# Kernel tuning notes

Measured on AMD Instinct MI355X. Metric: run time of the kernel, lower is better.

Reference implementation:

```python
import jax, jax.numpy as jnp
import numpy as np

K = 3  # spatial window (window_size = [1,3,3,1])


def _extract_patches(x, k):
    """TF-style extract_patches, VALID padding, stride 1, rate 1.
    x: [B,H,W,C] -> [B,Ho,Wo,k*k*C] with depth ordering (ki, kj, c)."""
    B, H, W, C = x.shape
    Ho, Wo = H - k + 1, W - k + 1
    cols = [x[:, ki:ki + Ho, kj:kj + Wo, :] for ki in range(k) for kj in range(k)]
    return jnp.concatenate(cols, axis=-1)


def setup_inputs() -> dict:
    key = jax.random.key(0)
    k1, k2 = jax.random.split(key)
    x = jax.random.normal(k1, (8, 32, 32, 32), dtype=jnp.float32)
    # weight shape per build(): (1, 1, 1, K*K*C, filters) = (1,1,1,288,64)
    w = jax.random.normal(k2, (1, 1, 1, 3 * 3 * 32, 64), dtype=jnp.float32) * 0.05
    bias = jnp.zeros((64,), dtype=jnp.float32)
    return {"x": x, "w": w, "bias": bias}


def reference(x, w, bias):
    # patches: [B,Ho,Wo,KKC]
    p = _extract_patches(x, K)
    # broadcast add: [B,Ho,Wo,KKC,1] + [KKC,F] -> [B,Ho,Wo,KKC,F]
    r = p[..., None] + w[0, 0, 0]
    # tropical conv: max-plus minus min-plus over the patch axis, plus bias
    return jnp.max(r, axis=3) - jnp.min(r, axis=3) + bias
```

## Files before the change

### kernel.cpp

```cpp
#include <hip/hip_runtime.h>
#include <math.h>


typedef _Float16 half2v __attribute__((ext_vector_type(2)));
typedef _Float16 half4v __attribute__((ext_vector_type(4)));

#define WSTRIDE 296

__device__ __forceinline__ void tap(half2v a, half2v& mx, half2v& mn) {
  mx = __builtin_elementwise_max(mx, a);
  mn = __builtin_elementwise_min(mn, a);
}

__device__ __forceinline__ half2v h2(unsigned u) {
  return __builtin_bit_cast(half2v, u);
}
__device__ __forceinline__ unsigned u32(half2v h) {
  return __builtin_bit_cast(unsigned, h);
}

__global__ __launch_bounds__(1024) void trop_kernel(
    const float* __restrict__ x, const float* __restrict__ w,
    const float* __restrict__ bias, float* __restrict__ out) {
  __shared__ _Float16 wt[64 * WSTRIDE];
  __shared__ _Float16 xh[3 * 32 * 32];
  __shared__ uint4 red[8][2][64];

  const int i = blockIdx.x;
  const int b = blockIdx.y;
  const int tid = threadIdx.x;
  const int f = tid & 63;
  const int W = __builtin_amdgcn_readfirstlane(tid >> 6);
  const int j0 = (W & 7) * 4;
  const int chalf = W >> 3;

  const int q = tid >> 6;
#pragma unroll
  for (int it = 0; it < 5; ++it) {
    int qq = q + it * 16;
    if (qq < 72) {
      int k0 = qq * 4;
      const float* wp = w + (size_t)k0 * 64 + f;
      half4v hv;
      hv.x = (_Float16)wp[0 * 64];
      hv.y = (_Float16)wp[1 * 64];
      hv.z = (_Float16)wp[2 * 64];
      hv.w = (_Float16)wp[3 * 64];
      *(half4v*)&wt[f * WSTRIDE + k0] = hv;
    }
  }

  const float* xb = x + (((size_t)b * 32 + i) * 32) * 32;
#pragma unroll
  for (int t = 0; t < 2; ++t) {
    int g = tid + t * 1024;
    if (g < 1536) {
      int ki = g >> 9;
      int rem = g & 511;
      int col = rem >> 4;
      int cp = rem & 15;
      float2 v = *(const float2*)(xb + ki * 1024 + col * 32 + cp * 2);
      half2v h;
      h.x = (_Float16)v.x;
      h.y = (_Float16)v.y;
      *(half2v*)&xh[(ki * 32 + col) * 32 + cp * 2] = h;
    }
  }

  __syncthreads();

  const int cc0 = ((j0 + 0 < 32) ? j0 + 0 : 31) * 32;
  const int cc1 = ((j0 + 1 < 32) ? j0 + 1 : 31) * 32;
  const int cc2 = ((j0 + 2 < 32) ? j0 + 2 : 31) * 32;
  const int cc3 = ((j0 + 3 < 32) ? j0 + 3 : 31) * 32;
  const int cc4 = ((j0 + 4 < 32) ? j0 + 4 : 31) * 32;
  const int cc5 = ((j0 + 5 < 32) ? j0 + 5 : 31) * 32;

  const _Float16 NI = (_Float16)(-INFINITY), PI = (_Float16)INFINITY;
  half2v mx0 = {NI, NI}, mx1 = {NI, NI}, mx2 = {NI, NI}, mx3 = {NI, NI};
  half2v mn0 = {PI, PI}, mn1 = {PI, PI}, mn2 = {PI, PI}, mn3 = {PI, PI};

#pragma clang loop unroll(disable)
  for (int kc = 0; kc < 6; ++kc) {
    const int ki = kc >> 1;
    const int c8 = ((kc & 1) << 3) + (chalf << 4);
    const _Float16* xrow = &xh[ki * 1024 + c8];
    const _Float16* wrow = &wt[f * WSTRIDE + ki * 96 + c8];

    uint4 xa0 = *(const uint4*)&xrow[cc0];
    uint4 xa1 = *(const uint4*)&xrow[cc1];
    uint4 xa2 = *(const uint4*)&xrow[cc2];
    uint4 xa3 = *(const uint4*)&xrow[cc3];
    uint4 xa4 = *(const uint4*)&xrow[cc4];
    uint4 xa5 = *(const uint4*)&xrow[cc5];
    uint4 wa0 = *(const uint4*)&wrow[0];
    uint4 wa1 = *(const uint4*)&wrow[32];
    uint4 wa2 = *(const uint4*)&wrow[64];

#define DOD(D)                                               \
  {                                                          \
    half2v w0 = h2(wa0.D);                                   \
    half2v w1 = h2(wa1.D);                                   \
    half2v w2 = h2(wa2.D);                                   \
    half2v x0 = h2(xa0.D);                                   \
    half2v x1 = h2(xa1.D);                                   \
    half2v x2 = h2(xa2.D);                                   \
    half2v x3 = h2(xa3.D);                                   \
    half2v x4 = h2(xa4.D);                                   \
    half2v x5 = h2(xa5.D);                                   \
    tap(x0 + w0, mx0, mn0); tap(x1 + w0, mx1, mn1);          \
    tap(x2 + w0, mx2, mn2); tap(x3 + w0, mx3, mn3);          \
    tap(x1 + w1, mx0, mn0); tap(x2 + w1, mx1, mn1);          \
    tap(x3 + w1, mx2, mn2); tap(x4 + w1, mx3, mn3);          \
    tap(x2 + w2, mx0, mn0); tap(x3 + w2, mx1, mn1);          \
    tap(x4 + w2, mx2, mn2); tap(x5 + w2, mx3, mn3);          \
  }
    DOD(x) DOD(y) DOD(z) DOD(w)
#undef DOD
  }

  if (W >= 8) {
    uint4 pm, pn;
    pm.x = u32(mx0); pm.y = u32(mx1); pm.z = u32(mx2); pm.w = u32(mx3);
    pn.x = u32(mn0); pn.y = u32(mn1); pn.z = u32(mn2); pn.w = u32(mn3);
    red[W - 8][0][f] = pm;
    red[W - 8][1][f] = pn;
  }
  __syncthreads();
  if (W < 8) {
    uint4 pm = red[W][0][f];
    uint4 pn = red[W][1][f];
    mx0 = __builtin_elementwise_max(mx0, h2(pm.x));
    mx1 = __builtin_elementwise_max(mx1, h2(pm.y));
    mx2 = __builtin_elementwise_max(mx2, h2(pm.z));
    mx3 = __builtin_elementwise_max(mx3, h2(pm.w));
    mn0 = __builtin_elementwise_min(mn0, h2(pn.x));
    mn1 = __builtin_elementwise_min(mn1, h2(pn.y));
    mn2 = __builtin_elementwise_min(mn2, h2(pn.z));
    mn3 = __builtin_elementwise_min(mn3, h2(pn.w));

    float bv = bias[f];
    float* ob = out + (((size_t)b * 30 + i) * 30 + j0) * 64 + f;
    if (j0 + 0 < 30) ob[0 * 64] = fmaxf((float)mx0.x, (float)mx0.y) - fminf((float)mn0.x, (float)mn0.y) + bv;
    if (j0 + 1 < 30) ob[1 * 64] = fmaxf((float)mx1.x, (float)mx1.y) - fminf((float)mn1.x, (float)mn1.y) + bv;
    if (j0 + 2 < 30) ob[2 * 64] = fmaxf((float)mx2.x, (float)mx2.y) - fminf((float)mn2.x, (float)mn2.y) + bv;
    if (j0 + 3 < 30) ob[3 * 64] = fmaxf((float)mx3.x, (float)mx3.y) - fminf((float)mn3.x, (float)mn3.y) + bv;
  }
}

extern "C" void kernel_launch(void* const* d_in, const int* in_sizes, int n_in,
                              void* d_out, int out_size, void* d_ws, size_t ws_size,
                              hipStream_t stream) {
  const float* x = (const float*)d_in[0];
  const float* w = (const float*)d_in[1];
  const float* bias = (const float*)d_in[2];
  float* out = (float*)d_out;
  dim3 grid(30, 8);
  dim3 block(1024);
  hipLaunchKernelGGL(trop_kernel, grid, block, 0, stream, x, w, bias, out);
}
```

Before: 65.22 us.

## Split output columns across grid z and use 256-thread blocks with 8 outputs per thread

The launch grows from 240 blocks of 1024 threads to 480 blocks of 256 threads, each block covering half the output columns. Each thread now accumulates 8 output columns instead of 4, which improves reuse of x loads from shared memory. Every block still loads and converts the full weight matrix to fp16, so global weight traffic and conversion work double. The cross-wave reduction shrinks from eight wave pairs to two.

```diff
diff --git a/kernel.cpp b/kernel.cpp
--- a/kernel.cpp
+++ b/kernel.cpp
@@ -3,14 +3,9 @@
 
 
 typedef _Float16 half2v __attribute__((ext_vector_type(2)));
-typedef _Float16 half4v __attribute__((ext_vector_type(4)));
+typedef _Float16 half8v __attribute__((ext_vector_type(8)));
 
 #define WSTRIDE 296
-
-__device__ __forceinline__ void tap(half2v a, half2v& mx, half2v& mn) {
-  mx = __builtin_elementwise_max(mx, a);
-  mn = __builtin_elementwise_min(mn, a);
-}
 
 __device__ __forceinline__ half2v h2(unsigned u) {
   return __builtin_bit_cast(half2v, u);
@@ -18,133 +13,145 @@
 __device__ __forceinline__ unsigned u32(half2v h) {
   return __builtin_bit_cast(unsigned, h);
 }
+__device__ __forceinline__ void tap(half2v a, half2v& mx, half2v& mn) {
+  mx = __builtin_elementwise_max(mx, a);
+  mn = __builtin_elementwise_min(mn, a);
+}
 
-__global__ __launch_bounds__(1024) void trop_kernel(
+__global__ __launch_bounds__(256, 3) void trop_kernel(
     const float* __restrict__ x, const float* __restrict__ w,
     const float* __restrict__ bias, float* __restrict__ out) {
   __shared__ _Float16 wt[64 * WSTRIDE];
-  __shared__ _Float16 xh[3 * 32 * 32];
-  __shared__ uint4 red[8][2][64];
+  __shared__ _Float16 xh[3 * 18 * 32];
+  __shared__ uint4 red[2][2][2][64];
 
   const int i = blockIdx.x;
   const int b = blockIdx.y;
+  const int z = blockIdx.z;
   const int tid = threadIdx.x;
   const int f = tid & 63;
   const int W = __builtin_amdgcn_readfirstlane(tid >> 6);
-  const int j0 = (W & 7) * 4;
-  const int chalf = W >> 3;
+  const int p = W & 1;
+  const int chalf = W >> 1;
+  const int j0 = z * 16 + p * 8;
 
-  const int q = tid >> 6;
+  {
+    const float* wp = w + f;
+    const int kb = W * 72;
 #pragma unroll
-  for (int it = 0; it < 5; ++it) {
-    int qq = q + it * 16;
-    if (qq < 72) {
-      int k0 = qq * 4;
-      const float* wp = w + (size_t)k0 * 64 + f;
-      half4v hv;
-      hv.x = (_Float16)wp[0 * 64];
-      hv.y = (_Float16)wp[1 * 64];
-      hv.z = (_Float16)wp[2 * 64];
-      hv.w = (_Float16)wp[3 * 64];
-      *(half4v*)&wt[f * WSTRIDE + k0] = hv;
+    for (int blk = 0; blk < 9; ++blk) {
+      const int k0 = kb + blk * 8;
+      half8v v;
+#pragma unroll
+      for (int u = 0; u < 8; ++u) v[u] = (_Float16)wp[(k0 + u) * 64];
+      *(half8v*)&wt[f * WSTRIDE + k0] = v;
     }
   }
 
-  const float* xb = x + (((size_t)b * 32 + i) * 32) * 32;
+  {
+    const float* xb = x + (((size_t)b * 32 + i) * 32) * 32;
 #pragma unroll
-  for (int t = 0; t < 2; ++t) {
-    int g = tid + t * 1024;
-    if (g < 1536) {
-      int ki = g >> 9;
-      int rem = g & 511;
-      int col = rem >> 4;
-      int cp = rem & 15;
-      float2 v = *(const float2*)(xb + ki * 1024 + col * 32 + cp * 2);
-      half2v h;
-      h.x = (_Float16)v.x;
-      h.y = (_Float16)v.y;
-      *(half2v*)&xh[(ki * 32 + col) * 32 + cp * 2] = h;
+    for (int t = 0; t < 4; ++t) {
+      const int g = tid + t * 256;
+      if (g < 864) {
+        const int ki = g / 288;
+        const int rem = g - ki * 288;
+        const int col = rem >> 4;
+        const int cp = rem & 15;
+        int gcol = z * 16 + col;
+        if (gcol > 31) gcol = 31;
+        const float2 v = *(const float2*)(xb + ki * 1024 + gcol * 32 + cp * 2);
+        half2v h;
+        h.x = (_Float16)v.x;
+        h.y = (_Float16)v.y;
+        *(half2v*)&xh[(ki * 18 + col) * 32 + cp * 2] = h;
+      }
     }
   }
 
   __syncthreads();
 
-  const int cc0 = ((j0 + 0 < 32) ? j0 + 0 : 31) * 32;
-  const int cc1 = ((j0 + 1 < 32) ? j0 + 1 : 31) * 32;
-  const int cc2 = ((j0 + 2 < 32) ? j0 + 2 : 31) * 32;
-  const int cc3 = ((j0 + 3 < 32) ? j0 + 3 : 31) * 32;
-  const int cc4 = ((j0 + 4 < 32) ? j0 + 4 : 31) * 32;
-  const int cc5 = ((j0 + 5 < 32) ? j0 + 5 : 31) * 32;
-
   const _Float16 NI = (_Float16)(-INFINITY), PI = (_Float16)INFINITY;
-  half2v mx0 = {NI, NI}, mx1 = {NI, NI}, mx2 = {NI, NI}, mx3 = {NI, NI};
-  half2v mn0 = {PI, PI}, mn1 = {PI, PI}, mn2 = {PI, PI}, mn3 = {PI, PI};
+  half2v mxi, mni;
+  mxi.x = NI; mxi.y = NI;
+  mni.x = PI; mni.y = PI;
+  half2v mx[8], mn[8];
+#pragma unroll
+  for (int t = 0; t < 8; ++t) {
+    mx[t] = mxi;
+    mn[t] = mni;
+  }
 
 #pragma clang loop unroll(disable)
   for (int kc = 0; kc < 6; ++kc) {
     const int ki = kc >> 1;
-    const int c8 = ((kc & 1) << 3) + (chalf << 4);
-    const _Float16* xrow = &xh[ki * 1024 + c8];
+    const int c8 = (chalf << 4) + ((kc & 1) << 3);
+    const _Float16* xrow = &xh[(ki * 18 + p * 8) * 32 + c8];
     const _Float16* wrow = &wt[f * WSTRIDE + ki * 96 + c8];
 
-    uint4 xa0 = *(const uint4*)&xrow[cc0];
-    uint4 xa1 = *(const uint4*)&xrow[cc1];
-    uint4 xa2 = *(const uint4*)&xrow[cc2];
-    uint4 xa3 = *(const uint4*)&xrow[cc3];
-    uint4 xa4 = *(const uint4*)&xrow[cc4];
-    uint4 xa5 = *(const uint4*)&xrow[cc5];
-    uint4 wa0 = *(const uint4*)&wrow[0];
-    uint4 wa1 = *(const uint4*)&wrow[32];
-    uint4 wa2 = *(const uint4*)&wrow[64];
+    uint4 xa[10];
+#pragma unroll
+    for (int t = 0; t < 10; ++t) xa[t] = *(const uint4*)&xrow[t * 32];
+    const uint4 wa0 = *(const uint4*)&wrow[0];
+    const uint4 wa1 = *(const uint4*)&wrow[32];
+    const uint4 wa2 = *(const uint4*)&wrow[64];
 
-#define DOD(D)                                               \
-  {                                                          \
-    half2v w0 = h2(wa0.D);                                   \
-    half2v w1 = h2(wa1.D);                                   \
-    half2v w2 = h2(wa2.D);                                   \
-    half2v x0 = h2(xa0.D);                                   \
-    half2v x1 = h2(xa1.D);                                   \
-    half2v x2 = h2(xa2.D);                                   \
-    half2v x3 = h2(xa3.D);                                   \
-    half2v x4 = h2(xa4.D);                                   \
-    half2v x5 = h2(xa5.D);                                   \
-    tap(x0 + w0, mx0, mn0); tap(x1 + w0, mx1, mn1);          \
-    tap(x2 + w0, mx2, mn2); tap(x3 + w0, mx3, mn3);          \
-    tap(x1 + w1, mx0, mn0); tap(x2 + w1, mx1, mn1);          \
-    tap(x3 + w1, mx2, mn2); tap(x4 + w1, mx3, mn3);          \
-    tap(x2 + w2, mx0, mn0); tap(x3 + w2, mx1, mn1);          \
-    tap(x4 + w2, mx2, mn2); tap(x5 + w2, mx3, mn3);          \
+#define DOD(D)                                      \
+  {                                                 \
+    const half2v w0 = h2(wa0.D);                    \
+    const half2v w1 = h2(wa1.D);                    \
+    const half2v w2 = h2(wa2.D);                    \
+    _Pragma("unroll") for (int t = 0; t < 8; ++t) { \
+      tap(h2(xa[t].D) + w0, mx[t], mn[t]);          \
+      tap(h2(xa[t + 1].D) + w1, mx[t], mn[t]);      \
+      tap(h2(xa[t + 2].D) + w2, mx[t], mn[t]);      \
+    }                                               \
   }
     DOD(x) DOD(y) DOD(z) DOD(w)
 #undef DOD
   }
 
-  if (W >= 8) {
-    uint4 pm, pn;
-    pm.x = u32(mx0); pm.y = u32(mx1); pm.z = u32(mx2); pm.w = u32(mx3);
-    pn.x = u32(mn0); pn.y = u32(mn1); pn.z = u32(mn2); pn.w = u32(mn3);
-    red[W - 8][0][f] = pm;
-    red[W - 8][1][f] = pn;
+  if (chalf == 1) {
+    uint4 t0, t1;
+    t0.x = u32(mx[0]); t0.y = u32(mx[1]); t0.z = u32(mx[2]); t0.w = u32(mx[3]);
+    t1.x = u32(mx[4]); t1.y = u32(mx[5]); t1.z = u32(mx[6]); t1.w = u32(mx[7]);
+    red[p][0][0][f] = t0;
+    red[p][0][1][f] = t1;
+    t0.x = u32(mn[0]); t0.y = u32(mn[1]); t0.z = u32(mn[2]); t0.w = u32(mn[3]);
+    t1.x = u32(mn[4]); t1.y = u32(mn[5]); t1.z = u32(mn[6]); t1.w = u32(mn[7]);
+    red[p][1][0][f] = t0;
+    red[p][1][1][f] = t1;
   }
   __syncthreads();
-  if (W < 8) {
-    uint4 pm = red[W][0][f];
-    uint4 pn = red[W][1][f];
-    mx0 = __builtin_elementwise_max(mx0, h2(pm.x));
-    mx1 = __builtin_elementwise_max(mx1, h2(pm.y));
-    mx2 = __builtin_elementwise_max(mx2, h2(pm.z));
-    mx3 = __builtin_elementwise_max(mx3, h2(pm.w));
-    mn0 = __builtin_elementwise_min(mn0, h2(pn.x));
-    mn1 = __builtin_elementwise_min(mn1, h2(pn.y));
-    mn2 = __builtin_elementwise_min(mn2, h2(pn.z));
-    mn3 = __builtin_elementwise_min(mn3, h2(pn.w));
+  if (chalf == 0) {
+    const uint4 a0 = red[p][0][0][f], a1 = red[p][0][1][f];
+    const uint4 b0 = red[p][1][0][f], b1 = red[p][1][1][f];
+    mx[0] = __builtin_elementwise_max(mx[0], h2(a0.x));
+    mx[1] = __builtin_elementwise_max(mx[1], h2(a0.y));
+    mx[2] = __builtin_elementwise_max(mx[2], h2(a0.z));
+    mx[3] = __builtin_elementwise_max(mx[3], h2(a0.w));
+    mx[4] = __builtin_elementwise_max(mx[4], h2(a1.x));
+    mx[5] = __builtin_elementwise_max(mx[5], h2(a1.y));
+    mx[6] = __builtin_elementwise_max(mx[6], h2(a1.z));
+    mx[7] = __builtin_elementwise_max(mx[7], h2(a1.w));
+    mn[0] = __builtin_elementwise_min(mn[0], h2(b0.x));
+    mn[1] = __builtin_elementwise_min(mn[1], h2(b0.y));
+    mn[2] = __builtin_elementwise_min(mn[2], h2(b0.z));
+    mn[3] = __builtin_elementwise_min(mn[3], h2(b0.w));
+    mn[4] = __builtin_elementwise_min(mn[4], h2(b1.x));
+    mn[5] = __builtin_elementwise_min(mn[5], h2(b1.y));
+    mn[6] = __builtin_elementwise_min(mn[6], h2(b1.z));
+    mn[7] = __builtin_elementwise_min(mn[7], h2(b1.w));
 
-    float bv = bias[f];
+    const float bv = bias[f];
     float* ob = out + (((size_t)b * 30 + i) * 30 + j0) * 64 + f;
-    if (j0 + 0 < 30) ob[0 * 64] = fmaxf((float)mx0.x, (float)mx0.y) - fminf((float)mn0.x, (float)mn0.y) + bv;
-    if (j0 + 1 < 30) ob[1 * 64] = fmaxf((float)mx1.x, (float)mx1.y) - fminf((float)mn1.x, (float)mn1.y) + bv;
-    if (j0 + 2 < 30) ob[2 * 64] = fmaxf((float)mx2.x, (float)mx2.y) - fminf((float)mn2.x, (float)mn2.y) + bv;
-    if (j0 + 3 < 30) ob[3 * 64] = fmaxf((float)mx3.x, (float)mx3.y) - fminf((float)mn3.x, (float)mn3.y) + bv;
+#pragma unroll
+    for (int t = 0; t < 8; ++t) {
+      if (j0 + t < 30) {
+        ob[t * 64] = fmaxf((float)mx[t].x, (float)mx[t].y) -
+                     fminf((float)mn[t].x, (float)mn[t].y) + bv;
+      }
+    }
   }
 }
 
@@ -155,7 +162,7 @@
   const float* w = (const float*)d_in[1];
   const float* bias = (const float*)d_in[2];
   float* out = (float*)d_out;
-  dim3 grid(30, 8);
-  dim3 block(1024);
+  dim3 grid(30, 8, 2);
+  dim3 block(256);
   hipLaunchKernelGGL(trop_kernel, grid, block, 0, stream, x, w, bias, out);
 }
```

New measurement: 68.71 us. 5.4% more time.
